# Optimization experiments

Measured on AMD Instinct MI355X. Metric: run time of the kernel, lower is better.

## Reference

```python
import jax, jax.numpy as jnp
import numpy as np

N_NODES = 100000
N_EDGES = 3200000
DIM = 64


def setup_inputs() -> dict:
    key = jax.random.key(0)
    k1, k2, k3, k4 = jax.random.split(key, 4)
    features = jax.random.normal(k1, (N_NODES, DIM), dtype=jnp.float32)
    attn_w = jax.random.normal(k2, (2 * DIM,), dtype=jnp.float32) / np.sqrt(2 * DIM)
    src = jax.random.randint(k3, (N_EDGES,), 0, N_NODES, dtype=jnp.int32)
    dst = jax.random.randint(k4, (N_EDGES,), 0, N_NODES, dtype=jnp.int32)
    return {"features": features, "attn_w": attn_w, "src": src, "dst": dst}


def reference(features, attn_w, src, dst):
    n = features.shape[0]
    d = features.shape[1]
    a_src, a_dst = attn_w[:d], attn_w[d:]
    # Edge attention: leaky_relu(Linear(concat(h_src, h_dst))) == leaky_relu(h_src@a_src + h_dst@a_dst)
    s_src = features @ a_src  # [N]
    s_dst = features @ a_dst  # [N]
    e = jax.nn.leaky_relu(s_src[src] + s_dst[dst], negative_slope=0.01)  # [E]
    # Segment softmax over incoming edges of each destination node
    emax = jax.ops.segment_max(e, dst, num_segments=n)  # [N], -inf for isolated nodes
    ee = jnp.exp(e - emax[dst])  # [E]
    denom = jax.ops.segment_sum(ee, dst, num_segments=n)  # [N]
    alpha = ee / denom[dst]  # [E]
    # Weighted neighbor aggregation (gather src feats, scatter-add into dst)
    h = jax.ops.segment_sum(alpha[:, None] * features[src], dst, num_segments=n)  # [N, D]
    return jax.nn.elu(h)
```

## Files before the change

### kernel.cpp

```cpp
#include <hip/hip_runtime.h>
#include <math.h>

#define DIM 64
#define SCAN_BLOCK 1024
#define NB1 1024
#define TPB2 1024
#define BUCKET_BITS 7
#define BUCKET_SZ 128
#define FB_SZ 64
#define SRC_SHIFT 20
#define CAP 6144
#define CAP2 2560
#define CHUNK 12500
#define STAGE_SZ 12544
#define NSPAN 784
#define RGRP 6

__device__ __forceinline__ float lrelu(float x) { return x > 0.f ? x : 0.01f * x; }
__device__ __forceinline__ float elu(float x)  { return x > 0.f ? x : expm1f(x); }

__global__ __launch_bounds__(TPB2)
void prep_scatter(const float* __restrict__ feat,
                  const float* __restrict__ attn_w,
                  float* __restrict__ s_src,
                  float* __restrict__ s_dst,
                  unsigned short* __restrict__ fbf,
                  int n_nodes,
                  const int* __restrict__ src,
                  const int* __restrict__ dst,
                  int* __restrict__ gcur,
                  int* __restrict__ bpk, int m, int nsb) {
    __shared__ int lh[NB1];
    __shared__ int bnd[NB1];
    __shared__ int cur[NB1];
    __shared__ int span_b[NSPAN];
    __shared__ int stage[STAGE_SZ];
    if (blockIdx.x < nsb) {
        int t = threadIdx.x;
        int lo = blockIdx.x * CHUNK;
        int hi = min(m, lo + CHUNK);
        int cc = hi - lo;
        int cc4 = cc >> 2;
        int nbux = (n_nodes + BUCKET_SZ - 1) >> BUCKET_BITS;
        const int4* dstv = reinterpret_cast<const int4*>(dst + lo);
        const int4* srcv = reinterpret_cast<const int4*>(src + lo);
        lh[t] = 0;
        __syncthreads();
        for (int i = t; i < cc4; i += TPB2) {
            int4 d = dstv[i];
            atomicAdd(&lh[d.x >> BUCKET_BITS], 1);
            atomicAdd(&lh[d.y >> BUCKET_BITS], 1);
            atomicAdd(&lh[d.z >> BUCKET_BITS], 1);
            atomicAdd(&lh[d.w >> BUCKET_BITS], 1);
        }
        for (int i = (cc4 << 2) + t; i < cc; i += TPB2)
            atomicAdd(&lh[dst[lo + i] >> BUCKET_BITS], 1);
        __syncthreads();
        cur[t] = lh[t];
        __syncthreads();
        for (int off = 1; off < NB1; off <<= 1) {
            int u = (t >= off) ? cur[t - off] : 0;
            __syncthreads();
            cur[t] += u;
            __syncthreads();
        }
        int excl = cur[t] - lh[t];
        bnd[t] = excl;
        int c = lh[t];
        int gb = (c > 0) ? atomicAdd(&gcur[t], c) : 0;
        lh[t]  = gb;
        cur[t] = excl;
        __syncthreads();
        if (t < nbux) {
            int s0 = (bnd[t] + 15) >> 4;
            int s1 = (bnd[t + 1] + 15) >> 4;
            for (int s = s0; s < s1; ++s) span_b[s] = t;
        }
        for (int i = t; i < cc4; i += TPB2) {
            int4 d = dstv[i];
            int4 s = srcv[i];
            int p0 = atomicAdd(&cur[d.x >> BUCKET_BITS], 1);
            stage[p0] = s.x | ((d.x & (BUCKET_SZ - 1)) << SRC_SHIFT);
            int p1 = atomicAdd(&cur[d.y >> BUCKET_BITS], 1);
            stage[p1] = s.y | ((d.y & (BUCKET_SZ - 1)) << SRC_SHIFT);
            int p2 = atomicAdd(&cur[d.z >> BUCKET_BITS], 1);
            stage[p2] = s.z | ((d.z & (BUCKET_SZ - 1)) << SRC_SHIFT);
            int p3 = atomicAdd(&cur[d.w >> BUCKET_BITS], 1);
            stage[p3] = s.w | ((d.w & (BUCKET_SZ - 1)) << SRC_SHIFT);
        }
        for (int i = (cc4 << 2) + t; i < cc; i += TPB2) {
            int d = dst[lo + i];
            int p = atomicAdd(&cur[d >> BUCKET_BITS], 1);
            stage[p] = src[lo + i] | ((d & (BUCKET_SZ - 1)) << SRC_SHIFT);
        }
        __syncthreads();
        for (int j = t; j < cc; j += TPB2) {
            int bkt = span_b[j >> 4];
            while (bnd[bkt + 1] <= j) ++bkt;
            int pos = lh[bkt] + (j - bnd[bkt]);
            if (pos < CAP)
                bpk[(size_t)bkt * CAP + pos] = stage[j];
        }
        return;
    }
    int gid  = (blockIdx.x - nsb) * blockDim.x + threadIdx.x;
    int node = gid >> 4;
    int lane = gid & 15;
    if (node >= n_nodes) return;
    const float4 f  = *reinterpret_cast<const float4*>(feat + (size_t)node * DIM + lane * 4);
    const float4 as = *reinterpret_cast<const float4*>(attn_w + lane * 4);
    const float4 ad = *reinterpret_cast<const float4*>(attn_w + DIM + lane * 4);
    float ps = f.x * as.x + f.y * as.y + f.z * as.z + f.w * as.w;
    float pd = f.x * ad.x + f.y * ad.y + f.z * ad.z + f.w * ad.w;
    uint b0 = __float_as_uint(f.x), b1 = __float_as_uint(f.y);
    uint b2 = __float_as_uint(f.z), b3 = __float_as_uint(f.w);
    ushort4 h;
    h.x = (unsigned short)((b0 + 0x7FFFu + ((b0 >> 16) & 1u)) >> 16);
    h.y = (unsigned short)((b1 + 0x7FFFu + ((b1 >> 16) & 1u)) >> 16);
    h.z = (unsigned short)((b2 + 0x7FFFu + ((b2 >> 16) & 1u)) >> 16);
    h.w = (unsigned short)((b3 + 0x7FFFu + ((b3 >> 16) & 1u)) >> 16);
    *reinterpret_cast<ushort4*>(fbf + (size_t)node * DIM + lane * 4) = h;
    for (int off = 8; off >= 1; off >>= 1) {
        ps += __shfl_xor(ps, off, 16);
        pd += __shfl_xor(pd, off, 16);
    }
    if (lane == 0) {
        s_src[node] = ps;
        s_dst[node] = pd;
    }
}

__device__ __forceinline__ void bf16x8_acc(uint4 q, float w,
                                           float& a0, float& a1, float& a2, float& a3,
                                           float& a4, float& a5, float& a6, float& a7) {
    a0 += w * __uint_as_float(q.x << 16);
    a1 += w * __uint_as_float(q.x & 0xffff0000u);
    a2 += w * __uint_as_float(q.y << 16);
    a3 += w * __uint_as_float(q.y & 0xffff0000u);
    a4 += w * __uint_as_float(q.z << 16);
    a5 += w * __uint_as_float(q.z & 0xffff0000u);
    a6 += w * __uint_as_float(q.w << 16);
    a7 += w * __uint_as_float(q.w & 0xffff0000u);
}

__global__ __launch_bounds__(256)
void sort_aggregate64(const int* __restrict__ bpk,
                      const int* __restrict__ gcur,
                      const float* __restrict__ s_src,
                      const float* __restrict__ s_dst,
                      const unsigned short* __restrict__ fbf,
                      float* __restrict__ out,
                      int n) {
    __shared__ float sdd[FB_SZ];
    __shared__ int   hist[FB_SZ];
    __shared__ int   offsl[FB_SZ];
    __shared__ int   cur[FB_SZ];
    __shared__ int   sA[FB_SZ];
    __shared__ int   sB[FB_SZ];
    __shared__ int   esrc_l[CAP2];
    __shared__ float w_l[CAP2];
    int f = blockIdx.x, t = threadIdx.x;
    int cb = f >> 1;
    int hb = (f & 1) << 6;
    int base = f * FB_SZ;
    int cnt = min(gcur[cb], CAP);
    const int*  bp  = bpk + (size_t)cb * CAP;
    const uint4* bp4 = reinterpret_cast<const uint4*>(bp);
    int cnt4 = cnt >> 2;
    uint4 rv[RGRP];
#pragma unroll
    for (int i = 0; i < RGRP; ++i) {
        int e = t + (i << 8);
        if (e < cnt4) rv[i] = bp4[e];
    }
    int tpk = 0;
    int te  = (cnt4 << 2) + t;
    bool ht = (te < cnt);
    if (ht) tpk = bp[te];
    if (t < FB_SZ) {
        hist[t] = 0;
        int nd = base + t;
        sdd[t] = (nd < n) ? s_dst[nd] : 0.f;
    }
    __syncthreads();
#define HPROC(pk) { int dl7_ = ((int)(pk) >> SRC_SHIFT) & 127; \
    if ((dl7_ & 64) == hb) atomicAdd(&hist[dl7_ & 63], 1); }
#pragma unroll
    for (int i = 0; i < RGRP; ++i) {
        int e = t + (i << 8);
        if (e < cnt4) {
            HPROC(rv[i].x) HPROC(rv[i].y) HPROC(rv[i].z) HPROC(rv[i].w)
        }
    }
    if (ht) HPROC(tpk)
    __syncthreads();
    if (t < FB_SZ) sA[t] = hist[t];
    __syncthreads();
    {
        int* pin = sA; int* pout = sB;
        for (int off = 1; off < FB_SZ; off <<= 1) {
            if (t < FB_SZ) pout[t] = (t >= off) ? pin[t] + pin[t - off] : pin[t];
            __syncthreads();
            int* tmpp = pin; pin = pout; pout = tmpp;
        }
        if (t < FB_SZ) {
            int excl = min(pin[t] - hist[t], CAP2);
            offsl[t] = excl;
            cur[t] = excl;
        }
    }
    __syncthreads();
#define SPROC(pk) { int dl7_ = ((int)(pk) >> SRC_SHIFT) & 127; \
    if ((dl7_ & 64) == hb) { \
        int sv_ = (int)(pk) & ((1 << SRC_SHIFT) - 1); \
        float w_ = __expf(lrelu(s_src[sv_] + sdd[dl7_ & 63])); \
        int p_ = atomicAdd(&cur[dl7_ & 63], 1); \
        if (p_ < CAP2) { esrc_l[p_] = sv_; w_l[p_] = w_; } } }
#pragma unroll
    for (int i = 0; i < RGRP; ++i) {
        int e = t + (i << 8);
        if (e < cnt4) {
            SPROC(rv[i].x) SPROC(rv[i].y) SPROC(rv[i].z) SPROC(rv[i].w)
        }
    }
    if (ht) SPROC(tpk)
    __syncthreads();
    int l8 = t & 7, grp = t >> 3;
    const uint4* fv4 = reinterpret_cast<const uint4*>(fbf);
    for (int node = grp; node < FB_SZ; node += 32) {
        int st = offsl[node];
        int en = min(st + hist[node], CAP2);
        float a0 = 0.f, a1 = 0.f, a2 = 0.f, a3 = 0.f;
        float a4 = 0.f, a5 = 0.f, a6 = 0.f, a7 = 0.f;
        float wsum = 0.f;
        int e = st;
        for (; e + 4 <= en; e += 4) {
            int   s0 = esrc_l[e],     s1 = esrc_l[e + 1];
            int   s2 = esrc_l[e + 2], s3 = esrc_l[e + 3];
            float w0 = w_l[e],        w1 = w_l[e + 1];
            float w2 = w_l[e + 2],    w3 = w_l[e + 3];
            uint4 q0 = fv4[(size_t)s0 * 8 + l8];
            uint4 q1 = fv4[(size_t)s1 * 8 + l8];
            uint4 q2 = fv4[(size_t)s2 * 8 + l8];
            uint4 q3 = fv4[(size_t)s3 * 8 + l8];
            wsum += (w0 + w1) + (w2 + w3);
            bf16x8_acc(q0, w0, a0, a1, a2, a3, a4, a5, a6, a7);
            bf16x8_acc(q1, w1, a0, a1, a2, a3, a4, a5, a6, a7);
            bf16x8_acc(q2, w2, a0, a1, a2, a3, a4, a5, a6, a7);
            bf16x8_acc(q3, w3, a0, a1, a2, a3, a4, a5, a6, a7);
        }
        for (; e < en; e++) {
            int   s0 = esrc_l[e];
            float w0 = w_l[e];
            uint4 q0 = fv4[(size_t)s0 * 8 + l8];
            wsum += w0;
            bf16x8_acc(q0, w0, a0, a1, a2, a3, a4, a5, a6, a7);
        }
        int nd = base + node;
        if (nd < n) {
            float inv = (en > st) ? 1.f / wsum : 0.f;
            float4 o1, o2;
            o1.x = elu(a0 * inv); o1.y = elu(a1 * inv);
            o1.z = elu(a2 * inv); o1.w = elu(a3 * inv);
            o2.x = elu(a4 * inv); o2.y = elu(a5 * inv);
            o2.z = elu(a6 * inv); o2.w = elu(a7 * inv);
            float4* orow = reinterpret_cast<float4*>(out + (size_t)nd * DIM + l8 * 8);
            orow[0] = o1;
            orow[1] = o2;
        }
    }
#undef HPROC
#undef SPROC
}

__global__ void compute_scores(const float* __restrict__ feat,
                               const float* __restrict__ attn_w,
                               float* __restrict__ s_src,
                               float* __restrict__ s_dst,
                               int n_nodes) {
    int gid  = blockIdx.x * blockDim.x + threadIdx.x;
    int node = gid >> 4;
    int lane = gid & 15;
    if (node >= n_nodes) return;
    const float4 f  = *reinterpret_cast<const float4*>(feat + (size_t)node * DIM + lane * 4);
    const float4 as = *reinterpret_cast<const float4*>(attn_w + lane * 4);
    const float4 ad = *reinterpret_cast<const float4*>(attn_w + DIM + lane * 4);
    float ps = f.x * as.x + f.y * as.y + f.z * as.z + f.w * as.w;
    float pd = f.x * ad.x + f.y * ad.y + f.z * ad.z + f.w * ad.w;
    for (int off = 8; off >= 1; off >>= 1) {
        ps += __shfl_xor(ps, off, 16);
        pd += __shfl_xor(pd, off, 16);
    }
    if (lane == 0) { s_src[node] = ps; s_dst[node] = pd; }
}

__global__ void scan_level1(const int* __restrict__ in, int* __restrict__ out,
                            int* __restrict__ bsum, int n) {
    __shared__ int tmp[SCAN_BLOCK];
    int t = threadIdx.x;
    int g = blockIdx.x * SCAN_BLOCK + t;
    int v = (g < n) ? in[g] : 0;
    tmp[t] = v;
    __syncthreads();
    for (int off = 1; off < SCAN_BLOCK; off <<= 1) {
        int u = (t >= off) ? tmp[t - off] : 0;
        __syncthreads();
        tmp[t] += u;
        __syncthreads();
    }
    if (g < n) out[g] = tmp[t] - v;
    if (t == SCAN_BLOCK - 1) bsum[blockIdx.x] = tmp[t];
}

__global__ void scan_level2(int* __restrict__ bsum, int nb) {
    __shared__ int tmp[SCAN_BLOCK];
    int t = threadIdx.x;
    int v = (t < nb) ? bsum[t] : 0;
    tmp[t] = v;
    __syncthreads();
    for (int off = 1; off < SCAN_BLOCK; off <<= 1) {
        int u = (t >= off) ? tmp[t - off] : 0;
        __syncthreads();
        tmp[t] += u;
        __syncthreads();
    }
    if (t < nb) bsum[t] = tmp[t] - v;
}

__global__ void scan_level3(int* __restrict__ out, const int* __restrict__ bsum,
                            int n) {
    int g = blockIdx.x * SCAN_BLOCK + threadIdx.x;
    if (g < n) out[g] += bsum[blockIdx.x];
}

__global__ void degree_rank(const int* __restrict__ dst, int* __restrict__ deg,
                            int* __restrict__ rank, int m) {
    int i = blockIdx.x * blockDim.x + threadIdx.x;
    if (i >= m) return;
    rank[i] = atomicAdd(&deg[dst[i]], 1);
}

__global__ void scatter_src(const int* __restrict__ src, const int* __restrict__ dst,
                            const int* __restrict__ rank, const int* __restrict__ offs,
                            int* __restrict__ esrc, int m) {
    int i = blockIdx.x * blockDim.x + threadIdx.x;
    if (i >= m) return;
    esrc[offs[dst[i]] + rank[i]] = src[i];
}

__global__ void aggregate_f32(const int* __restrict__ esrc,
                              const int* __restrict__ offs,
                              const int* __restrict__ deg,
                              const float* __restrict__ s_src,
                              const float* __restrict__ s_dst,
                              const float* __restrict__ feat,
                              float* __restrict__ out, int n) {
    int gid  = blockIdx.x * blockDim.x + threadIdx.x;
    int node = gid >> 4;
    int lane = gid & 15;
    if (node >= n) return;
    int start = offs[node];
    int cnt   = deg[node];
    float sdd = s_dst[node];
    const float4* fv = reinterpret_cast<const float4*>(feat);
    float4 acc = {0.f, 0.f, 0.f, 0.f};
    float wsum = 0.f;
    for (int e = 0; e < cnt; e++) {
        int s0 = esrc[start + e];
        float w0 = __expf(lrelu(s_src[s0] + sdd));
        float4 f0 = fv[s0 * 16 + lane];
        wsum += w0;
        acc.x += w0 * f0.x; acc.y += w0 * f0.y;
        acc.z += w0 * f0.z; acc.w += w0 * f0.w;
    }
    float inv = (cnt > 0) ? 1.f / wsum : 0.f;
    float4 o;
    o.x = elu(acc.x * inv); o.y = elu(acc.y * inv);
    o.z = elu(acc.z * inv); o.w = elu(acc.w * inv);
    reinterpret_cast<float4*>(out)[node * 16 + lane] = o;
}

extern "C" void kernel_launch(void* const* d_in, const int* in_sizes, int n_in,
                              void* d_out, int out_size, void* d_ws, size_t ws_size,
                              hipStream_t stream) {
    const float* feat   = (const float*)d_in[0];
    const float* attn_w = (const float*)d_in[1];
    const int*   src    = (const int*)d_in[2];
    const int*   dst    = (const int*)d_in[3];

    const int n = in_sizes[0] / DIM;
    const int m = in_sizes[2];

    float* out = (float*)d_out;

    const int nbux = (n + BUCKET_SZ - 1) >> BUCKET_BITS;
    const int nfb  = (n + FB_SZ - 1) / FB_SZ;

    float* s_src = (float*)d_ws;
    float* s_dst = s_src + n;
    unsigned short* fbf = (unsigned short*)(s_dst + n);
    int*   gcur  = (int*)(fbf + (size_t)n * DIM);
    int*   bpk   = gcur + NB1;
    size_t need  = ((size_t)(2 + DIM / 2) * n + NB1 + (size_t)nbux * CAP)
                   * sizeof(int);

    if (ws_size >= need && nbux <= NB1) {
        hipMemsetAsync(gcur, 0, (size_t)NB1 * sizeof(int), stream);

        int nsb = (m + CHUNK - 1) / CHUNK;
        int PB  = (n * 16 + TPB2 - 1) / TPB2;
        prep_scatter<<<nsb + PB, TPB2, 0, stream>>>(
            feat, attn_w, s_src, s_dst, fbf, n, src, dst, gcur, bpk, m, nsb);

        sort_aggregate64<<<nfb, 256, 0, stream>>>(
            bpk, gcur, s_src, s_dst, fbf, out, n);
    } else {
        int* deg2  = (int*)(s_dst + n);
        int* offs2 = deg2 + n;
        int* bsum2 = offs2 + n;
        int* rank  = bsum2 + SCAN_BLOCK;
        int* esr2  = rank + m;
        int threads = n * 16;
        compute_scores<<<(threads + 255) / 256, 256, 0, stream>>>(
            feat, attn_w, s_src, s_dst, n);
        hipMemsetAsync(deg2, 0, (size_t)n * sizeof(int), stream);
        degree_rank<<<(m + 255) / 256, 256, 0, stream>>>(dst, deg2, rank, m);
        int nb2 = (n + SCAN_BLOCK - 1) / SCAN_BLOCK;
        scan_level1<<<nb2, SCAN_BLOCK, 0, stream>>>(deg2, offs2, bsum2, n);
        scan_level2<<<1, SCAN_BLOCK, 0, stream>>>(bsum2, nb2);
        scan_level3<<<nb2, SCAN_BLOCK, 0, stream>>>(offs2, bsum2, n);
        scatter_src<<<(m + 255) / 256, 256, 0, stream>>>(src, dst, rank, offs2, esr2, m);
        aggregate_f32<<<(threads + 255) / 256, 256, 0, stream>>>(
            esr2, offs2, deg2, s_src, s_dst, feat, out, n);
    }
}
```

Baseline: 173.3 us.

## Register-cache edge chunk and replace block scan with wave shuffle scan

The bucket-scatter blocks now load each thread's dst/src int4 values once into registers up front, up to four per thread. Both the histogram pass and the staging pass reuse those registers instead of re-reading global memory twice. The 1024-entry Hillis-Steele shared-memory scan, with its roughly twenty barriers, is replaced by a wavefront shuffle scan plus a 16-entry cross-wave scan. This relies on CHUNK/4 fitting in four register slots per thread and raises register pressure.

Result: slower. 177.3 us (+2.3%).

```diff
diff --git a/kernel.cpp b/kernel.cpp
--- a/kernel.cpp
+++ b/kernel.cpp
@@ -14,6 +14,7 @@
 #define CHUNK 12500
 #define STAGE_SZ 12544
 #define NSPAN 784
+#define RG1 4
 #define RGRP 6
 
 __device__ __forceinline__ float lrelu(float x) { return x > 0.f ? x : 0.01f * x; }
@@ -33,6 +34,7 @@
     __shared__ int lh[NB1];
     __shared__ int bnd[NB1];
     __shared__ int cur[NB1];
+    __shared__ int wsc[16];
     __shared__ int span_b[NSPAN];
     __shared__ int stage[STAGE_SZ];
     if (blockIdx.x < nsb) {
@@ -44,29 +46,53 @@
         int nbux = (n_nodes + BUCKET_SZ - 1) >> BUCKET_BITS;
         const int4* dstv = reinterpret_cast<const int4*>(dst + lo);
         const int4* srcv = reinterpret_cast<const int4*>(src + lo);
+        int4 rd[RG1], rs[RG1];
+#pragma unroll
+        for (int i = 0; i < RG1; ++i) {
+            int e = t + (i << 10);
+            if (e < cc4) { rd[i] = dstv[e]; rs[i] = srcv[e]; }
+        }
+        int tdst = 0, tsrc = 0;
+        int te = (cc4 << 2) + t;
+        bool ht = (te < cc);
+        if (ht) { tdst = dst[lo + te]; tsrc = src[lo + te]; }
         lh[t] = 0;
         __syncthreads();
-        for (int i = t; i < cc4; i += TPB2) {
-            int4 d = dstv[i];
-            atomicAdd(&lh[d.x >> BUCKET_BITS], 1);
-            atomicAdd(&lh[d.y >> BUCKET_BITS], 1);
-            atomicAdd(&lh[d.z >> BUCKET_BITS], 1);
-            atomicAdd(&lh[d.w >> BUCKET_BITS], 1);
-        }
-        for (int i = (cc4 << 2) + t; i < cc; i += TPB2)
-            atomicAdd(&lh[dst[lo + i] >> BUCKET_BITS], 1);
-        __syncthreads();
-        cur[t] = lh[t];
-        __syncthreads();
-        for (int off = 1; off < NB1; off <<= 1) {
-            int u = (t >= off) ? cur[t - off] : 0;
-            __syncthreads();
-            cur[t] += u;
-            __syncthreads();
-        }
-        int excl = cur[t] - lh[t];
+#pragma unroll
+        for (int i = 0; i < RG1; ++i) {
+            int e = t + (i << 10);
+            if (e < cc4) {
+                atomicAdd(&lh[rd[i].x >> BUCKET_BITS], 1);
+                atomicAdd(&lh[rd[i].y >> BUCKET_BITS], 1);
+                atomicAdd(&lh[rd[i].z >> BUCKET_BITS], 1);
+                atomicAdd(&lh[rd[i].w >> BUCKET_BITS], 1);
+            }
+        }
+        if (ht) atomicAdd(&lh[tdst >> BUCKET_BITS], 1);
+        __syncthreads();
+        int c = lh[t];
+        int lane = t & 63, wid = t >> 6;
+        int x = c;
+#pragma unroll
+        for (int off = 1; off < 64; off <<= 1) {
+            int u = __shfl_up(x, off, 64);
+            if (lane >= off) x += u;
+        }
+        if (lane == 63) wsc[wid] = x;
+        __syncthreads();
+        if (t < 16) {
+            int y = wsc[t];
+#pragma unroll
+            for (int off = 1; off < 16; off <<= 1) {
+                int u = __shfl_up(y, off, 16);
+                if (t >= off) y += u;
+            }
+            wsc[t] = y;
+        }
+        __syncthreads();
+        int wbase = (wid > 0) ? wsc[wid - 1] : 0;
+        int excl = wbase + x - c;
         bnd[t] = excl;
-        int c = lh[t];
         int gb = (c > 0) ? atomicAdd(&gcur[t], c) : 0;
         lh[t]  = gb;
         cur[t] = excl;
@@ -76,22 +102,23 @@
             int s1 = (bnd[t + 1] + 15) >> 4;
             for (int s = s0; s < s1; ++s) span_b[s] = t;
         }
-        for (int i = t; i < cc4; i += TPB2) {
-            int4 d = dstv[i];
-            int4 s = srcv[i];
-            int p0 = atomicAdd(&cur[d.x >> BUCKET_BITS], 1);
-            stage[p0] = s.x | ((d.x & (BUCKET_SZ - 1)) << SRC_SHIFT);
-            int p1 = atomicAdd(&cur[d.y >> BUCKET_BITS], 1);
-            stage[p1] = s.y | ((d.y & (BUCKET_SZ - 1)) << SRC_SHIFT);
-            int p2 = atomicAdd(&cur[d.z >> BUCKET_BITS], 1);
-            stage[p2] = s.z | ((d.z & (BUCKET_SZ - 1)) << SRC_SHIFT);
-            int p3 = atomicAdd(&cur[d.w >> BUCKET_BITS], 1);
-            stage[p3] = s.w | ((d.w & (BUCKET_SZ - 1)) << SRC_SHIFT);
-        }
-        for (int i = (cc4 << 2) + t; i < cc; i += TPB2) {
-            int d = dst[lo + i];
-            int p = atomicAdd(&cur[d >> BUCKET_BITS], 1);
-            stage[p] = src[lo + i] | ((d & (BUCKET_SZ - 1)) << SRC_SHIFT);
+#pragma unroll
+        for (int i = 0; i < RG1; ++i) {
+            int e = t + (i << 10);
+            if (e < cc4) {
+                int p0 = atomicAdd(&cur[rd[i].x >> BUCKET_BITS], 1);
+                stage[p0] = rs[i].x | ((rd[i].x & (BUCKET_SZ - 1)) << SRC_SHIFT);
+                int p1 = atomicAdd(&cur[rd[i].y >> BUCKET_BITS], 1);
+                stage[p1] = rs[i].y | ((rd[i].y & (BUCKET_SZ - 1)) << SRC_SHIFT);
+                int p2 = atomicAdd(&cur[rd[i].z >> BUCKET_BITS], 1);
+                stage[p2] = rs[i].z | ((rd[i].z & (BUCKET_SZ - 1)) << SRC_SHIFT);
+                int p3 = atomicAdd(&cur[rd[i].w >> BUCKET_BITS], 1);
+                stage[p3] = rs[i].w | ((rd[i].w & (BUCKET_SZ - 1)) << SRC_SHIFT);
+            }
+        }
+        if (ht) {
+            int p = atomicAdd(&cur[tdst >> BUCKET_BITS], 1);
+            stage[p] = tsrc | ((tdst & (BUCKET_SZ - 1)) << SRC_SHIFT);
         }
         __syncthreads();
         for (int j = t; j < cc; j += TPB2) {
```
